# Kernel tuning notes

Measured on AMD Instinct MI355X. Metric: run time of the kernel, lower is better.

The kernel has to match this reference:

```python
import jax, jax.numpy as jnp
import numpy as np

N_NODES = 50000
N_EDGES = 800000
NODE_DIM = 128
EDGE_DIM = 32
HIDDEN = 128
OUT_DIM = 128


def _linear_params(key, fan_in, fan_out):
    k1, k2 = jax.random.split(key)
    bound = 1.0 / np.sqrt(fan_in)
    W = jax.random.uniform(k1, (fan_in, fan_out), minval=-bound, maxval=bound, dtype=jnp.float32)
    b = jax.random.uniform(k2, (fan_out,), minval=-bound, maxval=bound, dtype=jnp.float32)
    return W, b


def setup_inputs() -> dict:
    key = jax.random.key(0)
    ks = jax.random.split(key, 7)
    h = jax.random.normal(ks[0], (N_NODES, NODE_DIM), dtype=jnp.float32)
    edge_index = jax.random.randint(ks[1], (2, N_EDGES), 0, N_NODES, dtype=jnp.int64)
    edge_attr = jax.random.normal(ks[2], (N_EDGES, EDGE_DIM), dtype=jnp.float32)
    We1, be1 = _linear_params(ks[3], 2 * NODE_DIM + EDGE_DIM, HIDDEN)
    We2, be2 = _linear_params(ks[4], HIDDEN, HIDDEN)
    Wh1, bh1 = _linear_params(ks[5], NODE_DIM + HIDDEN, HIDDEN)
    Wh2, bh2 = _linear_params(ks[6], HIDDEN, OUT_DIM)
    return {"h": h, "edge_index": edge_index, "edge_attr": edge_attr,
            "We1": We1, "be1": be1, "We2": We2, "be2": be2,
            "Wh1": Wh1, "bh1": bh1, "Wh2": Wh2, "bh2": bh2}


def _mlp(x, W1, b1, W2, b2):
    return jax.nn.relu(x @ W1 + b1) @ W2 + b2


def reference(h, edge_index, edge_attr, We1, be1, We2, be2, Wh1, bh1, Wh2, bh2):
    src = edge_index[0]
    dst = edge_index[1]
    # gather endpoint features and concat with edge attributes: [E, 2*D+De]
    edge_input = jnp.concatenate([h[src], h[dst], edge_attr], axis=-1)
    m_ij = _mlp(edge_input, We1, be1, We2, be2)  # [E, H]
    # scatter-add messages into destination nodes
    m_i = jax.ops.segment_sum(m_ij, dst, num_segments=h.shape[0])  # [N, H]
    node_input = jnp.concatenate([h, m_i], axis=-1)  # [N, D+H]
    h_next = _mlp(node_input, Wh1, bh1, Wh2, bh2)  # [N, out]
    return h_next
```

## Files before the change

kernel.cpp:

```cpp
#include <hip/hip_runtime.h>

#define E_TOTAL 800000
#define N_TOTAL 50000
#define NBINS   50176

typedef __attribute__((ext_vector_type(8))) short short8;
typedef __attribute__((ext_vector_type(4))) float floatx4;

__device__ __forceinline__ unsigned short f2bf(float f) {
    union { float f; unsigned u; } x; x.f = f;
    unsigned r = x.u + 0x7fff + ((x.u >> 16) & 1);
    return (unsigned short)(r >> 16);
}

__device__ __forceinline__ void gload_lds16(const void* g, void* l) {
    __builtin_amdgcn_global_load_lds(
        (const __attribute__((address_space(1))) void*)g,
        (__attribute__((address_space(3))) void*)l, 16, 0, 0);
}
__device__ __forceinline__ void gload_lds4(const void* g, void* l) {
    __builtin_amdgcn_global_load_lds(
        (const __attribute__((address_space(1))) void*)g,
        (__attribute__((address_space(3))) void*)l, 4, 0, 0);
}

__global__ __launch_bounds__(256)
void prep(const float* __restrict__ We1, const float* __restrict__ We2,
          const float* __restrict__ Wh1, const float* __restrict__ Wh2,
          unsigned short* __restrict__ W1t, unsigned short* __restrict__ W2t,
          unsigned short* __restrict__ Wh1t, unsigned short* __restrict__ Wh2t,
          const float* __restrict__ h, unsigned short* __restrict__ hbf,
          int do_cvt, int do_sort,
          float* __restrict__ mi, int* __restrict__ hist)
{
    const int b = blockIdx.x;
    const int tid = threadIdx.x;
    if (b < 400) {
        int t = b * 256 + tid;
        if (t < 36864) {
            W1t[(t & 127) * 288 + (t >> 7)] = f2bf(We1[t]);
        } else if (t < 53248) {
            t -= 36864;
            W2t[(t & 127) * 128 + (t >> 7)] = f2bf(We2[t]);
        } else if (t < 86016) {
            t -= 53248;
            Wh1t[(t & 127) * 256 + (t >> 7)] = f2bf(Wh1[t]);
        } else if (t < 102400) {
            t -= 86016;
            Wh2t[(t & 127) * 128 + (t >> 7)] = f2bf(Wh2[t]);
        }
    } else if (b < 6650) {
        const int t = (b - 400) * 256 + tid;
        ((float4*)mi)[t] = make_float4(0.f, 0.f, 0.f, 0.f);
    } else if (b < 9775) {
        if (do_cvt) {
            const int t = (b - 6650) * 256 + tid;
            const float4* h4 = (const float4*)h;
            float4 a = h4[(size_t)t * 2];
            float4 c = h4[(size_t)t * 2 + 1];
            short8 v = { (short)f2bf(a.x), (short)f2bf(a.y), (short)f2bf(a.z), (short)f2bf(a.w),
                         (short)f2bf(c.x), (short)f2bf(c.y), (short)f2bf(c.z), (short)f2bf(c.w) };
            *(short8*)(&hbf[(size_t)t * 8]) = v;
        }
    } else {
        if (do_sort) hist[(b - 9775) * 256 + tid] = 0;
    }
}

__global__ __launch_bounds__(256) void k_hist(const int* __restrict__ ei, int* __restrict__ hist) {
    const int t = blockIdx.x * 256 + threadIdx.x;
    atomicAdd(&hist[ei[E_TOTAL + t]], 1);
}
__global__ __launch_bounds__(256) void k_scan1(const int* __restrict__ hist, int* __restrict__ partial) {
    __shared__ int s[256];
    s[threadIdx.x] = hist[blockIdx.x * 256 + threadIdx.x];
    __syncthreads();
    for (int off = 128; off > 0; off >>= 1) {
        if (threadIdx.x < off) s[threadIdx.x] += s[threadIdx.x + off];
        __syncthreads();
    }
    if (threadIdx.x == 0) partial[blockIdx.x] = s[0];
}
__global__ __launch_bounds__(256)
void k_scan2(const int* __restrict__ partial, int* __restrict__ partialOff) {
    __shared__ int s[256];
    const int t = threadIdx.x;
    const int NP = NBINS / 256;
    const int v = (t < NP) ? partial[t] : 0;
    s[t] = v; __syncthreads();
    for (int off = 1; off < 256; off <<= 1) {
        int x = (t >= off) ? s[t - off] : 0;
        __syncthreads();
        s[t] += x;
        __syncthreads();
    }
    if (t < NP) partialOff[t] = s[t] - v;
}
__global__ __launch_bounds__(256)
void k_scan3(const int* __restrict__ hist, const int* __restrict__ partialOff,
             int* __restrict__ cursor) {
    __shared__ int s[256];
    const int t = threadIdx.x, g = blockIdx.x * 256 + t;
    const int v = hist[g];
    s[t] = v; __syncthreads();
    for (int off = 1; off < 256; off <<= 1) {
        int x = (t >= off) ? s[t - off] : 0;
        __syncthreads();
        s[t] += x;
        __syncthreads();
    }
    cursor[g] = partialOff[blockIdx.x] + s[t] - v;
}
__global__ __launch_bounds__(256)
void k_scatter(const int* __restrict__ ei, const float* __restrict__ ea,
               int* __restrict__ cursor,
               int* __restrict__ srcS, int* __restrict__ dstS,
               unsigned short* __restrict__ eabf) {
    const int t = blockIdx.x * 256 + threadIdx.x;
    const int src = ei[t];
    const int dst = ei[E_TOTAL + t];
    const int pos = atomicAdd(&cursor[dst], 1);
    srcS[pos] = src;
    dstS[pos] = dst;
    const float4* ea4 = (const float4*)ea;
    #pragma unroll
    for (int j = 0; j < 4; ++j) {
        float4 a = ea4[(size_t)t * 8 + j * 2];
        float4 b = ea4[(size_t)t * 8 + j * 2 + 1];
        short8 v = { (short)f2bf(a.x), (short)f2bf(a.y), (short)f2bf(a.z), (short)f2bf(a.w),
                     (short)f2bf(b.x), (short)f2bf(b.y), (short)f2bf(b.z), (short)f2bf(b.w) };
        *(short8*)(&eabf[(size_t)pos * 32 + j * 8]) = v;
    }
}

constexpr int XK = 296;
constexpr int HK = 136;
constexpr int NK = 264;
constexpr int FJ = 132;

#define MFMA8(A, B, C) { \
    C[0][0] = __builtin_amdgcn_mfma_f32_16x16x32_bf16(A[0], B[0], C[0][0], 0, 0, 0); \
    C[0][1] = __builtin_amdgcn_mfma_f32_16x16x32_bf16(A[0], B[1], C[0][1], 0, 0, 0); \
    C[1][0] = __builtin_amdgcn_mfma_f32_16x16x32_bf16(A[1], B[0], C[1][0], 0, 0, 0); \
    C[1][1] = __builtin_amdgcn_mfma_f32_16x16x32_bf16(A[1], B[1], C[1][1], 0, 0, 0); \
    C[2][0] = __builtin_amdgcn_mfma_f32_16x16x32_bf16(A[2], B[0], C[2][0], 0, 0, 0); \
    C[2][1] = __builtin_amdgcn_mfma_f32_16x16x32_bf16(A[2], B[1], C[2][1], 0, 0, 0); \
    C[3][0] = __builtin_amdgcn_mfma_f32_16x16x32_bf16(A[3], B[0], C[3][0], 0, 0, 0); \
    C[3][1] = __builtin_amdgcn_mfma_f32_16x16x32_bf16(A[3], B[1], C[3][1], 0, 0, 0); }

__global__ __launch_bounds__(256, 2)
void edge_mfma_sorted(const unsigned short* __restrict__ hbf,
                      const int* __restrict__ srcS,
                      const int* __restrict__ dstS,
                      const unsigned short* __restrict__ eabf,
                      const unsigned short* __restrict__ W1t,
                      const float* __restrict__ b1,
                      const unsigned short* __restrict__ W2t,
                      const float* __restrict__ b2,
                      float* __restrict__ mi)
{
    constexpr int NT = E_TOTAL / 64;
    constexpr int XH = 64 * 288;
    __shared__ alignas(16) unsigned short sMem[2 * XH + 768];
    int* idb = (int*)&sMem[2 * XH];

    const int tid  = threadIdx.x;
    const int lane = tid & 63;
    const int w    = tid >> 6;
    const int q    = lane >> 4;
    const int lr   = lane & 15;
    const int n0   = w * 32;
    const int q8   = q * 8;
    const int S    = (int)gridDim.x;

    const int w1b0 = (n0 + lr) * 288, w1b1 = (n0 + 16 + lr) * 288;
    const int w2b0 = (n0 + lr) * 128, w2b1 = (n0 + 16 + lr) * 128;
    const int h0 = lr * HK, h1 = (16 + lr) * HK, h2 = (32 + lr) * HK, h3 = (48 + lr) * HK;

    const float bias1[2] = { b1[n0 + lr], b1[n0 + 16 + lr] };
    const float bias2[2] = { b2[n0 + lr], b2[n0 + 16 + lr] };

    auto ID_DMA = [&](int tt, int k) {
        if (w == 0)      gload_lds4(srcS + tt * 64 + lane, &idb[k * 128]);
        else if (w == 1) gload_lds4(dstS + tt * 64 + lane, &idb[k * 128 + 64]);
    };

    auto X_DMA = [&](int tt, int bufS, int k) {
        const int* ids = &idb[k * 128];
        #pragma unroll
        for (int j = 0; j < 9; ++j) {
            const int tj = j * 256 + tid;
            const int e  = tj / 36;
            const int p  = tj - e * 36;
            const int c  = (p < 32) ? (p ^ (e & 15)) : p;
            const int node = ids[((c & 16) ? 64 : 0) + e];
            const char* gh = (const char*)hbf + (size_t)node * 256 + (size_t)(c & 15) * 16;
            const char* ge = (const char*)eabf + ((size_t)tt * 64 + e) * 64 + (size_t)(p - 32) * 16;
            const void* g  = (p < 32) ? (const void*)gh : (const void*)ge;
            gload_lds16(g, (void*)&sMem[bufS + j * 2048 + w * 512]);
        }
    };

#define LA1(KS, A) { \
    const int cs = ((KS) < 8) ? ((((KS) * 4 + q) ^ lr) * 8) : ((32 + q) * 8); \
    A[0] = *(const short8*)(&sX[( 0 + lr) * 288 + cs]); \
    A[1] = *(const short8*)(&sX[(16 + lr) * 288 + cs]); \
    A[2] = *(const short8*)(&sX[(32 + lr) * 288 + cs]); \
    A[3] = *(const short8*)(&sX[(48 + lr) * 288 + cs]); }
#define LB1(KS, B) { B[0] = *(const short8*)(&W1t[w1b0 + (KS) * 32 + q8]); \
                     B[1] = *(const short8*)(&W1t[w1b1 + (KS) * 32 + q8]); }
#define LA2(KS, A) { A[0] = *(const short8*)(&sX[h0 + (KS) * 32 + q8]); \
                     A[1] = *(const short8*)(&sX[h1 + (KS) * 32 + q8]); \
                     A[2] = *(const short8*)(&sX[h2 + (KS) * 32 + q8]); \
                     A[3] = *(const short8*)(&sX[h3 + (KS) * 32 + q8]); }
#define LB2(KS, B) { B[0] = *(const short8*)(&W2t[w2b0 + (KS) * 32 + q8]); \
                     B[1] = *(const short8*)(&W2t[w2b1 + (KS) * 32 + q8]); }

    int t  = blockIdx.x;
    int cur = 0, ib = 0;

    ID_DMA(t, 0);
    ID_DMA(t + S, 1);
    __syncthreads();
    X_DMA(t, 0, 0);
    __syncthreads();

    while (t < NT) {
        unsigned short* sX = &sMem[cur * XH];

        const int t2 = t + 2 * S;
        if (t2 < NT) ID_DMA(t2, (ib + 2) % 3);
        const int tn = t + S;
        if (tn < NT) X_DMA(tn, (cur ^ 1) * XH, (ib + 1) % 3);

        floatx4 acc[4][2];
        #pragma unroll
        for (int mt = 0; mt < 4; ++mt)
            #pragma unroll
            for (int nt = 0; nt < 2; ++nt)
                acc[mt][nt] = (floatx4){0.f, 0.f, 0.f, 0.f};
        {
            short8 aX[4], aY[4], bX[2], bY[2];
            LB1(0, bX); LB1(1, bY); LA1(0, aX);
            LA1(1, aY); MFMA8(aX, bX, acc); LB1(2, bX);
            LA1(2, aX); MFMA8(aY, bY, acc); LB1(3, bY);
            LA1(3, aY); MFMA8(aX, bX, acc); LB1(4, bX);
            LA1(4, aX); MFMA8(aY, bY, acc); LB1(5, bY);
            LA1(5, aY); MFMA8(aX, bX, acc); LB1(6, bX);
            LA1(6, aX); MFMA8(aY, bY, acc); LB1(7, bY);
            LA1(7, aY); MFMA8(aX, bX, acc); LB1(8, bX);
            LA1(8, aX); MFMA8(aY, bY, acc);
            MFMA8(aX, bX, acc);
        }
        __syncthreads();

        {
            #pragma unroll
            for (int mt = 0; mt < 4; ++mt)
                #pragma unroll
                for (int nt = 0; nt < 2; ++nt)
                    #pragma unroll
                    for (int r = 0; r < 4; ++r) {
                        float v = fmaxf(acc[mt][nt][r] + bias1[nt], 0.f);
                        sX[(mt * 16 + q * 4 + r) * HK + n0 + nt * 16 + lr] = f2bf(v);
                    }
        }
        __syncthreads();

        floatx4 acc2[4][2];
        #pragma unroll
        for (int mt = 0; mt < 4; ++mt)
            #pragma unroll
            for (int nt = 0; nt < 2; ++nt)
                acc2[mt][nt] = (floatx4){0.f, 0.f, 0.f, 0.f};
        {
            short8 aX[4], aY[4], bX[2], bY[2];
            LB2(0, bX); LB2(1, bY); LA2(0, aX);
            LA2(1, aY); MFMA8(aX, bX, acc2); LB2(2, bX);
            LA2(2, aX); MFMA8(aY, bY, acc2); LB2(3, bY);
            LA2(3, aY); MFMA8(aX, bX, acc2);
            MFMA8(aY, bY, acc2);
        }
        __syncthreads();

        float* sF = (float*)sX;
        {
            #pragma unroll
            for (int mt = 0; mt < 4; ++mt)
                #pragma unroll
                for (int nt = 0; nt < 2; ++nt)
                    #pragma unroll
                    for (int r = 0; r < 4; ++r)
                        sF[(mt * 16 + q * 4 + r) * FJ + n0 + nt * 16 + lr] =
                            acc2[mt][nt][r] + bias2[nt];
        }
        __syncthreads();

        {
            const int* idsDst = &idb[ib * 128 + 64];
            const int g  = tid >> 7;
            const int j  = tid & 127;
            const int r0 = g * 32;
            float sum = 0.f;
            for (int r = r0; r < r0 + 32; ++r) {
                sum += sF[r * FJ + j];
                const int dst = idsDst[r];
                if (r == r0 + 31 || idsDst[r + 1] != dst) {
                    atomicAdd(&mi[(size_t)dst * 128 + j], sum);
                    sum = 0.f;
                }
            }
        }
        __syncthreads();

        cur ^= 1;
        ib = (ib == 2) ? 0 : ib + 1;
        t = tn;
    }
#undef LA1
#undef LB1
#undef LA2
#undef LB2
}

template <bool PRECVT>
__global__ __launch_bounds__(256, 8)
void edge_mfma_flat(const float* __restrict__ h,
                    const unsigned short* __restrict__ hbf,
                    const int* __restrict__ ei,
                    const float* __restrict__ ea,
                    const unsigned short* __restrict__ W1t,
                    const float* __restrict__ b1,
                    const unsigned short* __restrict__ W2t,
                    const float* __restrict__ b2,
                    float* __restrict__ mi)
{
    __shared__ unsigned short sMem[32 * XK];
    __shared__ int sDst[32];

    const int tid = threadIdx.x;
    const int e0  = blockIdx.x * 32;
    if (tid < 32) sDst[tid] = ei[E_TOTAL + e0 + tid];

    const float4* h4   = (const float4*)h;
    const short8* hbf8 = (const short8*)hbf;
    const float4* ea4  = (const float4*)ea;
    #pragma unroll
    for (int it = 0; it < 5; ++it) {
        const int idx = tid + it * 256;
        const int e  = idx / 40;
        const int c  = idx - e * 40;
        const int ge = e0 + e;
        if (c < 32) {
            const int node = (c < 16) ? ei[ge] : ei[E_TOTAL + ge];
            const int cc = c & 15;
            short8 v;
            if (PRECVT) {
                v = hbf8[(size_t)node * 16 + cc];
            } else {
                float4 x = h4[(size_t)node * 32 + cc * 2];
                float4 y = h4[(size_t)node * 32 + cc * 2 + 1];
                v = (short8){ (short)f2bf(x.x), (short)f2bf(x.y), (short)f2bf(x.z), (short)f2bf(x.w),
                              (short)f2bf(y.x), (short)f2bf(y.y), (short)f2bf(y.z), (short)f2bf(y.w) };
            }
            *(short8*)(&sMem[e * XK + c * 8]) = v;
        } else {
            float4 x = ea4[(size_t)ge * 8 + (c - 32)];
            unsigned short* p = &sMem[e * XK + 128 + c * 4];
            p[0] = f2bf(x.x); p[1] = f2bf(x.y); p[2] = f2bf(x.z); p[3] = f2bf(x.w);
        }
    }
    __syncthreads();

    const int lane = tid & 63;
    const int w    = tid >> 6;
    const int q    = lane >> 4;
    const int lr   = lane & 15;
    const int n0   = w * 32;

    floatx4 acc[2][2];
    #pragma unroll
    for (int mt = 0; mt < 2; ++mt)
        #pragma unroll
        for (int nt = 0; nt < 2; ++nt)
            acc[mt][nt] = (floatx4){0.f, 0.f, 0.f, 0.f};
    #pragma unroll
    for (int ks = 0; ks < 9; ++ks) {
        const int kb = ks * 32 + q * 8;
        short8 a[2], b[2];
        #pragma unroll
        for (int mt = 0; mt < 2; ++mt)
            a[mt] = *(const short8*)(&sMem[(mt * 16 + lr) * XK + kb]);
        #pragma unroll
        for (int nt = 0; nt < 2; ++nt)
            b[nt] = *(const short8*)(&W1t[(n0 + nt * 16 + lr) * 288 + kb]);
        #pragma unroll
        for (int mt = 0; mt < 2; ++mt)
            #pragma unroll
            for (int nt = 0; nt < 2; ++nt)
                acc[mt][nt] = __builtin_amdgcn_mfma_f32_16x16x32_bf16(
                    a[mt], b[nt], acc[mt][nt], 0, 0, 0);
    }
    __syncthreads();
    {
        float bias[2] = { b1[n0 + lr], b1[n0 + 16 + lr] };
        #pragma unroll
        for (int mt = 0; mt < 2; ++mt)
            #pragma unroll
            for (int nt = 0; nt < 2; ++nt)
                #pragma unroll
                for (int r = 0; r < 4; ++r) {
                    float v = fmaxf(acc[mt][nt][r] + bias[nt], 0.f);
                    sMem[(mt * 16 + q * 4 + r) * HK + n0 + nt * 16 + lr] = f2bf(v);
                }
    }
    __syncthreads();
    floatx4 acc2[2][2];
    #pragma unroll
    for (int mt = 0; mt < 2; ++mt)
        #pragma unroll
        for (int nt = 0; nt < 2; ++nt)
            acc2[mt][nt] = (floatx4){0.f, 0.f, 0.f, 0.f};
    #pragma unroll
    for (int ks = 0; ks < 4; ++ks) {
        const int kb = ks * 32 + q * 8;
        short8 a[2], b[2];
        #pragma unroll
        for (int mt = 0; mt < 2; ++mt)
            a[mt] = *(const short8*)(&sMem[(mt * 16 + lr) * HK + kb]);
        #pragma unroll
        for (int nt = 0; nt < 2; ++nt)
            b[nt] = *(const short8*)(&W2t[(n0 + nt * 16 + lr) * 128 + kb]);
        #pragma unroll
        for (int mt = 0; mt < 2; ++mt)
            #pragma unroll
            for (int nt = 0; nt < 2; ++nt)
                acc2[mt][nt] = __builtin_amdgcn_mfma_f32_16x16x32_bf16(
                    a[mt], b[nt], acc2[mt][nt], 0, 0, 0);
    }
    {
        float bias[2] = { b2[n0 + lr], b2[n0 + 16 + lr] };
        #pragma unroll
        for (int mt = 0; mt < 2; ++mt)
            #pragma unroll
            for (int r = 0; r < 4; ++r) {
                const int m   = mt * 16 + q * 4 + r;
                const int dst = sDst[m];
                float* row = &mi[(size_t)dst * 128];
                #pragma unroll
                for (int nt = 0; nt < 2; ++nt)
                    atomicAdd(&row[n0 + nt * 16 + lr], acc2[mt][nt][r] + bias[nt]);
            }
    }
}

template <bool USEHBF>
__global__ __launch_bounds__(256, 8)
void node_mfma(const float* __restrict__ h,
               const unsigned short* __restrict__ hbf,
               const float* __restrict__ mi,
               const unsigned short* __restrict__ W1t,
               const float* __restrict__ b1,
               const unsigned short* __restrict__ W2t,
               const float* __restrict__ b2,
               float* __restrict__ out)
{
    __shared__ unsigned short sMem[32 * NK];

    const int tid = threadIdx.x;
    const int g0  = blockIdx.x * 32;

    const float4* h4   = (const float4*)h;
    const short8* hbf8 = (const short8*)hbf;
    const float4* mi4  = (const float4*)mi;
    if (USEHBF) {
        #pragma unroll
        for (int it = 0; it < 2; ++it) {
            const int idx = tid + it * 256;
            const int n  = idx >> 4;
            const int c  = idx & 15;
            const int gn = g0 + n;
            short8 v = (short8){0,0,0,0,0,0,0,0};
            if (gn < N_TOTAL) v = hbf8[(size_t)gn * 16 + c];
            *(short8*)(&sMem[n * NK + c * 8]) = v;
        }
        #pragma unroll
        for (int it = 0; it < 4; ++it) {
            const int idx = tid + it * 256;
            const int n  = idx >> 5;
            const int c  = idx & 31;
            const int gn = g0 + n;
            float4 v = make_float4(0.f, 0.f, 0.f, 0.f);
            if (gn < N_TOTAL) v = mi4[(size_t)gn * 32 + c];
            unsigned short* p = &sMem[n * NK + 128 + c * 4];
            p[0] = f2bf(v.x); p[1] = f2bf(v.y); p[2] = f2bf(v.z); p[3] = f2bf(v.w);
        }
    } else {
        #pragma unroll
        for (int it = 0; it < 8; ++it) {
            const int idx = tid + it * 256;
            const int n  = idx >> 6;
            const int c  = idx & 63;
            const int gn = g0 + n;
            float4 v = make_float4(0.f, 0.f, 0.f, 0.f);
            if (gn < N_TOTAL)
                v = (c < 32) ? h4[(size_t)gn * 32 + c] : mi4[(size_t)gn * 32 + (c - 32)];
            unsigned short* p = &sMem[n * NK + c * 4];
            p[0] = f2bf(v.x); p[1] = f2bf(v.y); p[2] = f2bf(v.z); p[3] = f2bf(v.w);
        }
    }
    __syncthreads();

    const int lane = tid & 63;
    const int w    = tid >> 6;
    const int q    = lane >> 4;
    const int lr   = lane & 15;
    const int n0   = w * 32;

    floatx4 acc[2][2];
    #pragma unroll
    for (int mt = 0; mt < 2; ++mt)
        #pragma unroll
        for (int nt = 0; nt < 2; ++nt)
            acc[mt][nt] = (floatx4){0.f, 0.f, 0.f, 0.f};
    #pragma unroll
    for (int ks = 0; ks < 8; ++ks) {
        const int kb = ks * 32 + q * 8;
        short8 a[2], b[2];
        #pragma unroll
        for (int mt = 0; mt < 2; ++mt)
            a[mt] = *(const short8*)(&sMem[(mt * 16 + lr) * NK + kb]);
        #pragma unroll
        for (int nt = 0; nt < 2; ++nt)
            b[nt] = *(const short8*)(&W1t[(n0 + nt * 16 + lr) * 256 + kb]);
        #pragma unroll
        for (int mt = 0; mt < 2; ++mt)
            #pragma unroll
            for (int nt = 0; nt < 2; ++nt)
                acc[mt][nt] = __builtin_amdgcn_mfma_f32_16x16x32_bf16(
                    a[mt], b[nt], acc[mt][nt], 0, 0, 0);
    }
    __syncthreads();
    {
        float bias[2] = { b1[n0 + lr], b1[n0 + 16 + lr] };
        #pragma unroll
        for (int mt = 0; mt < 2; ++mt)
            #pragma unroll
            for (int nt = 0; nt < 2; ++nt)
                #pragma unroll
                for (int r = 0; r < 4; ++r) {
                    float v = fmaxf(acc[mt][nt][r] + bias[nt], 0.f);
                    sMem[(mt * 16 + q * 4 + r) * HK + n0 + nt * 16 + lr] = f2bf(v);
                }
    }
    __syncthreads();
    floatx4 acc2[2][2];
    #pragma unroll
    for (int mt = 0; mt < 2; ++mt)
        #pragma unroll
        for (int nt = 0; nt < 2; ++nt)
            acc2[mt][nt] = (floatx4){0.f, 0.f, 0.f, 0.f};
    #pragma unroll
    for (int ks = 0; ks < 4; ++ks) {
        const int kb = ks * 32 + q * 8;
        short8 a[2], b[2];
        #pragma unroll
        for (int mt = 0; mt < 2; ++mt)
            a[mt] = *(const short8*)(&sMem[(mt * 16 + lr) * HK + kb]);
        #pragma unroll
        for (int nt = 0; nt < 2; ++nt)
            b[nt] = *(const short8*)(&W2t[(n0 + nt * 16 + lr) * 128 + kb]);
        #pragma unroll
        for (int mt = 0; mt < 2; ++mt)
            #pragma unroll
            for (int nt = 0; nt < 2; ++nt)
                acc2[mt][nt] = __builtin_amdgcn_mfma_f32_16x16x32_bf16(
                    a[mt], b[nt], acc2[mt][nt], 0, 0, 0);
    }
    {
        float bias[2] = { b2[n0 + lr], b2[n0 + 16 + lr] };
        #pragma unroll
        for (int mt = 0; mt < 2; ++mt)
            #pragma unroll
            for (int r = 0; r < 4; ++r) {
                const int gm = g0 + mt * 16 + q * 4 + r;
                if (gm < N_TOTAL) {
                    #pragma unroll
                    for (int nt = 0; nt < 2; ++nt)
                        out[(size_t)gm * 128 + n0 + nt * 16 + lr] =
                            acc2[mt][nt][r] + bias[nt];
                }
            }
    }
}

extern "C" void kernel_launch(void* const* d_in, const int* in_sizes, int n_in,
                              void* d_out, int out_size, void* d_ws, size_t ws_size,
                              hipStream_t stream) {
    const float* h   = (const float*)d_in[0];
    const int*   ei  = (const int*)d_in[1];
    const float* ea  = (const float*)d_in[2];
    const float* We1 = (const float*)d_in[3];
    const float* be1 = (const float*)d_in[4];
    const float* We2 = (const float*)d_in[5];
    const float* be2 = (const float*)d_in[6];
    const float* Wh1 = (const float*)d_in[7];
    const float* bh1 = (const float*)d_in[8];
    const float* Wh2 = (const float*)d_in[9];
    const float* bh2 = (const float*)d_in[10];
    float* out = (float*)d_out;

    const size_t szMi   = (size_t)N_TOTAL * 128 * sizeof(float);
    const size_t szW1t  = 128 * 288 * 2;
    const size_t szW2t  = 128 * 128 * 2;
    const size_t szWh1t = 128 * 256 * 2;
    const size_t szWh2t = 128 * 128 * 2;
    const size_t szHbf  = (size_t)N_TOTAL * 128 * 2;
    const size_t szIds  = (size_t)E_TOTAL * 4;
    const size_t szEabf = (size_t)E_TOTAL * 32 * 2;
    const size_t szHist = (size_t)NBINS * 4;

    const size_t offW1t  = szMi;
    const size_t offW2t  = offW1t + szW1t;
    const size_t offWh1t = offW2t + szW2t;
    const size_t offWh2t = offWh1t + szWh1t;
    const size_t offHbf  = offWh2t + szWh2t;
    const size_t offSrc  = offHbf + szHbf;
    const size_t offDst  = offSrc + szIds;
    const size_t offEabf = offDst + szIds;
    const size_t offHist = offEabf + szEabf;
    const size_t offCur  = offHist + szHist;
    const size_t offP1   = offCur + szHist;
    const size_t offP2   = offP1 + 1024;
    const size_t needFull = offP2 + 1024;
    const size_t needCvt  = offSrc;

    char* wsb = (char*)d_ws;
    float* mi = (float*)wsb;
    unsigned short* W1t  = (unsigned short*)(wsb + offW1t);
    unsigned short* W2t  = (unsigned short*)(wsb + offW2t);
    unsigned short* Wh1t = (unsigned short*)(wsb + offWh1t);
    unsigned short* Wh2t = (unsigned short*)(wsb + offWh2t);
    unsigned short* hbf  = (unsigned short*)(wsb + offHbf);
    int* srcS    = (int*)(wsb + offSrc);
    int* dstS    = (int*)(wsb + offDst);
    unsigned short* eabf = (unsigned short*)(wsb + offEabf);
    int* hist    = (int*)(wsb + offHist);
    int* cursor  = (int*)(wsb + offCur);
    int* partial = (int*)(wsb + offP1);
    int* poff    = (int*)(wsb + offP2);

    const int full   = (ws_size >= needFull) ? 1 : 0;
    const int do_cvt = (ws_size >= needCvt + szHbf) ? 1 : 0;

    prep<<<9971, 256, 0, stream>>>(We1, We2, Wh1, Wh2, W1t, W2t, Wh1t, Wh2t,
                                   h, hbf, do_cvt, full, mi, hist);

    if (full) {
        k_hist<<<E_TOTAL / 256, 256, 0, stream>>>(ei, hist);
        k_scan1<<<NBINS / 256, 256, 0, stream>>>(hist, partial);
        k_scan2<<<1, 256, 0, stream>>>(partial, poff);
        k_scan3<<<NBINS / 256, 256, 0, stream>>>(hist, poff, cursor);
        k_scatter<<<E_TOTAL / 256, 256, 0, stream>>>(ei, ea, cursor, srcS, dstS, eabf);
        edge_mfma_sorted<<<512, 256, 0, stream>>>(
            hbf, srcS, dstS, eabf, W1t, be1, W2t, be2, mi);
        node_mfma<true><<<(N_TOTAL + 31) / 32, 256, 0, stream>>>(
            h, hbf, mi, Wh1t, bh1, Wh2t, bh2, out);
    } else if (do_cvt) {
        edge_mfma_flat<true><<<E_TOTAL / 32, 256, 0, stream>>>(
            h, hbf, ei, ea, W1t, be1, W2t, be2, mi);
        node_mfma<true><<<(N_TOTAL + 31) / 32, 256, 0, stream>>>(
            h, hbf, mi, Wh1t, bh1, Wh2t, bh2, out);
    } else {
        edge_mfma_flat<false><<<E_TOTAL / 32, 256, 0, stream>>>(
            h, nullptr, ei, ea, W1t, be1, W2t, be2, mi);
        node_mfma<false><<<(N_TOTAL + 31) / 32, 256, 0, stream>>>(
            h, nullptr, mi, Wh1t, bh1, Wh2t, bh2, out);
    }
    (void)in_sizes; (void)n_in; (void)out_size;
}
```

Baseline: 443.4 us.

## Use 8 waves per block in sorted edge kernel, 16 output columns each

Doubles the edge MLP kernel's block size from 256 to 512 threads. Each of the 8 waves now computes a 16-column slice of the hidden output instead of 32, with the gather DMA, epilogue and segmented atomic reduction rebalanced across the larger block. The aim is more waves per CU to hide gather latency and spread the per-tile work, at the cost of each wave re-reading the A tile from LDS, since A-operand LDS traffic per tile doubles. Launch bounds now request 4 blocks of 512 threads per CU, which tightens the register budget.

```diff
diff --git a/kernel.cpp b/kernel.cpp
--- a/kernel.cpp
+++ b/kernel.cpp
@@ -148,7 +148,13 @@
     C[3][0] = __builtin_amdgcn_mfma_f32_16x16x32_bf16(A[3], B[0], C[3][0], 0, 0, 0); \
     C[3][1] = __builtin_amdgcn_mfma_f32_16x16x32_bf16(A[3], B[1], C[3][1], 0, 0, 0); }
 
-__global__ __launch_bounds__(256, 2)
+#define MFMA4(A, B, C) { \
+    C[0] = __builtin_amdgcn_mfma_f32_16x16x32_bf16(A[0], B, C[0], 0, 0, 0); \
+    C[1] = __builtin_amdgcn_mfma_f32_16x16x32_bf16(A[1], B, C[1], 0, 0, 0); \
+    C[2] = __builtin_amdgcn_mfma_f32_16x16x32_bf16(A[2], B, C[2], 0, 0, 0); \
+    C[3] = __builtin_amdgcn_mfma_f32_16x16x32_bf16(A[3], B, C[3], 0, 0, 0); }
+
+__global__ __launch_bounds__(512, 4)
 void edge_mfma_sorted(const unsigned short* __restrict__ hbf,
                       const int* __restrict__ srcS,
                       const int* __restrict__ dstS,
@@ -169,16 +175,16 @@
     const int w    = tid >> 6;
     const int q    = lane >> 4;
     const int lr   = lane & 15;
-    const int n0   = w * 32;
+    const int n0   = w * 16;
     const int q8   = q * 8;
     const int S    = (int)gridDim.x;
 
-    const int w1b0 = (n0 + lr) * 288, w1b1 = (n0 + 16 + lr) * 288;
-    const int w2b0 = (n0 + lr) * 128, w2b1 = (n0 + 16 + lr) * 128;
+    const int w1b = (n0 + lr) * 288;
+    const int w2b = (n0 + lr) * 128;
     const int h0 = lr * HK, h1 = (16 + lr) * HK, h2 = (32 + lr) * HK, h3 = (48 + lr) * HK;
 
-    const float bias1[2] = { b1[n0 + lr], b1[n0 + 16 + lr] };
-    const float bias2[2] = { b2[n0 + lr], b2[n0 + 16 + lr] };
+    const float bias1 = b1[n0 + lr];
+    const float bias2 = b2[n0 + lr];
 
     auto ID_DMA = [&](int tt, int k) {
         if (w == 0)      gload_lds4(srcS + tt * 64 + lane, &idb[k * 128]);
@@ -188,16 +194,18 @@
     auto X_DMA = [&](int tt, int bufS, int k) {
         const int* ids = &idb[k * 128];
         #pragma unroll
-        for (int j = 0; j < 9; ++j) {
-            const int tj = j * 256 + tid;
-            const int e  = tj / 36;
-            const int p  = tj - e * 36;
-            const int c  = (p < 32) ? (p ^ (e & 15)) : p;
-            const int node = ids[((c & 16) ? 64 : 0) + e];
-            const char* gh = (const char*)hbf + (size_t)node * 256 + (size_t)(c & 15) * 16;
-            const char* ge = (const char*)eabf + ((size_t)tt * 64 + e) * 64 + (size_t)(p - 32) * 16;
-            const void* g  = (p < 32) ? (const void*)gh : (const void*)ge;
-            gload_lds16(g, (void*)&sMem[bufS + j * 2048 + w * 512]);
+        for (int j = 0; j < 5; ++j) {
+            if (j < 4 || tid < 256) {
+                const int tj = j * 512 + tid;
+                const int e  = tj / 36;
+                const int p  = tj - e * 36;
+                const int c  = (p < 32) ? (p ^ (e & 15)) : p;
+                const int node = ids[((c & 16) ? 64 : 0) + e];
+                const char* gh = (const char*)hbf + (size_t)node * 256 + (size_t)(c & 15) * 16;
+                const char* ge = (const char*)eabf + ((size_t)tt * 64 + e) * 64 + (size_t)(p - 32) * 16;
+                const void* g  = (p < 32) ? (const void*)gh : (const void*)ge;
+                gload_lds16(g, (void*)&sMem[bufS + j * 4096 + w * 512]);
+            }
         }
     };
 
@@ -207,14 +215,12 @@
     A[1] = *(const short8*)(&sX[(16 + lr) * 288 + cs]); \
     A[2] = *(const short8*)(&sX[(32 + lr) * 288 + cs]); \
     A[3] = *(const short8*)(&sX[(48 + lr) * 288 + cs]); }
-#define LB1(KS, B) { B[0] = *(const short8*)(&W1t[w1b0 + (KS) * 32 + q8]); \
-                     B[1] = *(const short8*)(&W1t[w1b1 + (KS) * 32 + q8]); }
+#define LB1(KS, B) { B = *(const short8*)(&W1t[w1b + (KS) * 32 + q8]); }
 #define LA2(KS, A) { A[0] = *(const short8*)(&sX[h0 + (KS) * 32 + q8]); \
                      A[1] = *(const short8*)(&sX[h1 + (KS) * 32 + q8]); \
                      A[2] = *(const short8*)(&sX[h2 + (KS) * 32 + q8]); \
                      A[3] = *(const short8*)(&sX[h3 + (KS) * 32 + q8]); }
-#define LB2(KS, B) { B[0] = *(const short8*)(&W2t[w2b0 + (KS) * 32 + q8]); \
-                     B[1] = *(const short8*)(&W2t[w2b1 + (KS) * 32 + q8]); }
+#define LB2(KS, B) { B = *(const short8*)(&W2t[w2b + (KS) * 32 + q8]); }
 
     int t  = blockIdx.x;
     int cur = 0, ib = 0;
@@ -233,24 +239,22 @@
         const int tn = t + S;
         if (tn < NT) X_DMA(tn, (cur ^ 1) * XH, (ib + 1) % 3);
 
-        floatx4 acc[4][2];
+        floatx4 acc[4];
         #pragma unroll
         for (int mt = 0; mt < 4; ++mt)
-            #pragma unroll
-            for (int nt = 0; nt < 2; ++nt)
-                acc[mt][nt] = (floatx4){0.f, 0.f, 0.f, 0.f};
+            acc[mt] = (floatx4){0.f, 0.f, 0.f, 0.f};
         {
-            short8 aX[4], aY[4], bX[2], bY[2];
+            short8 aX[4], aY[4], bX, bY;
             LB1(0, bX); LB1(1, bY); LA1(0, aX);
-            LA1(1, aY); MFMA8(aX, bX, acc); LB1(2, bX);
-            LA1(2, aX); MFMA8(aY, bY, acc); LB1(3, bY);
-            LA1(3, aY); MFMA8(aX, bX, acc); LB1(4, bX);
-            LA1(4, aX); MFMA8(aY, bY, acc); LB1(5, bY);
-            LA1(5, aY); MFMA8(aX, bX, acc); LB1(6, bX);
-            LA1(6, aX); MFMA8(aY, bY, acc); LB1(7, bY);
-            LA1(7, aY); MFMA8(aX, bX, acc); LB1(8, bX);
-            LA1(8, aX); MFMA8(aY, bY, acc);
-            MFMA8(aX, bX, acc);
+            LA1(1, aY); MFMA4(aX, bX, acc); LB1(2, bX);
+            LA1(2, aX); MFMA4(aY, bY, acc); LB1(3, bY);
+            LA1(3, aY); MFMA4(aX, bX, acc); LB1(4, bX);
+            LA1(4, aX); MFMA4(aY, bY, acc); LB1(5, bY);
+            LA1(5, aY); MFMA4(aX, bX, acc); LB1(6, bX);
+            LA1(6, aX); MFMA4(aY, bY, acc); LB1(7, bY);
+            LA1(7, aY); MFMA4(aX, bX, acc); LB1(8, bX);
+            LA1(8, aX); MFMA4(aY, bY, acc);
+            MFMA4(aX, bX, acc);
         }
         __syncthreads();
 
@@ -258,28 +262,24 @@
             #pragma unroll
             for (int mt = 0; mt < 4; ++mt)
                 #pragma unroll
-                for (int nt = 0; nt < 2; ++nt)
-                    #pragma unroll
-                    for (int r = 0; r < 4; ++r) {
-                        float v = fmaxf(acc[mt][nt][r] + bias1[nt], 0.f);
-                        sX[(mt * 16 + q * 4 + r) * HK + n0 + nt * 16 + lr] = f2bf(v);
-                    }
-        }
-        __syncthreads();
-
-        floatx4 acc2[4][2];
+                for (int r = 0; r < 4; ++r) {
+                    float v = fmaxf(acc[mt][r] + bias1, 0.f);
+                    sX[(mt * 16 + q * 4 + r) * HK + n0 + lr] = f2bf(v);
+                }
+        }
+        __syncthreads();
+
+        floatx4 acc2[4];
         #pragma unroll
         for (int mt = 0; mt < 4; ++mt)
-            #pragma unroll
-            for (int nt = 0; nt < 2; ++nt)
-                acc2[mt][nt] = (floatx4){0.f, 0.f, 0.f, 0.f};
+            acc2[mt] = (floatx4){0.f, 0.f, 0.f, 0.f};
         {
-            short8 aX[4], aY[4], bX[2], bY[2];
+            short8 aX[4], aY[4], bX, bY;
             LB2(0, bX); LB2(1, bY); LA2(0, aX);
-            LA2(1, aY); MFMA8(aX, bX, acc2); LB2(2, bX);
-            LA2(2, aX); MFMA8(aY, bY, acc2); LB2(3, bY);
-            LA2(3, aY); MFMA8(aX, bX, acc2);
-            MFMA8(aY, bY, acc2);
+            LA2(1, aY); MFMA4(aX, bX, acc2); LB2(2, bX);
+            LA2(2, aX); MFMA4(aY, bY, acc2); LB2(3, bY);
+            LA2(3, aY); MFMA4(aX, bX, acc2);
+            MFMA4(aY, bY, acc2);
         }
         __syncthreads();
 
@@ -288,11 +288,8 @@
             #pragma unroll
             for (int mt = 0; mt < 4; ++mt)
                 #pragma unroll
-                for (int nt = 0; nt < 2; ++nt)
-                    #pragma unroll
-                    for (int r = 0; r < 4; ++r)
-                        sF[(mt * 16 + q * 4 + r) * FJ + n0 + nt * 16 + lr] =
-                            acc2[mt][nt][r] + bias2[nt];
+                for (int r = 0; r < 4; ++r)
+                    sF[(mt * 16 + q * 4 + r) * FJ + n0 + lr] = acc2[mt][r] + bias2;
         }
         __syncthreads();
 
@@ -300,12 +297,12 @@
             const int* idsDst = &idb[ib * 128 + 64];
             const int g  = tid >> 7;
             const int j  = tid & 127;
-            const int r0 = g * 32;
+            const int r0 = g * 16;
             float sum = 0.f;
-            for (int r = r0; r < r0 + 32; ++r) {
+            for (int r = r0; r < r0 + 16; ++r) {
                 sum += sF[r * FJ + j];
                 const int dst = idsDst[r];
-                if (r == r0 + 31 || idsDst[r + 1] != dst) {
+                if (r == r0 + 15 || idsDst[r + 1] != dst) {
                     atomicAdd(&mi[(size_t)dst * 128 + j], sum);
                     sum = 0.f;
                 }
@@ -662,7 +659,7 @@
         k_scan2<<<1, 256, 0, stream>>>(partial, poff);
         k_scan3<<<NBINS / 256, 256, 0, stream>>>(hist, poff, cursor);
         k_scatter<<<E_TOTAL / 256, 256, 0, stream>>>(ei, ea, cursor, srcS, dstS, eabf);
-        edge_mfma_sorted<<<512, 256, 0, stream>>>(
+        edge_mfma_sorted<<<512, 512, 0, stream>>>(
             hbf, srcS, dstS, eabf, W1t, be1, W2t, be2, mi);
         node_mfma<true><<<(N_TOTAL + 31) / 32, 256, 0, stream>>>(
             h, hbf, mi, Wh1t, bh1, Wh2t, bh2, out);
```

Result: slower. 483.7 us (+9.1%).

## Split edge tile across eight waves with 2x4 wave grid per block

Applied to the files above, without the earlier changes.

Doubles the edge kernel block size to 512 threads. Waves are arranged as 2 row groups by 4 column groups, so each wave computes a 32x32 output tile instead of 64x32. The gather DMA and the segmented scatter-add loop are re-partitioned to match: 5 DMA rounds, and 16-row segments across 4 thread groups. This is meant to add latency hiding through more waves per block. In exchange, each weight fragment is loaded twice per tile, shorter segments issue more atomics, and the tighter launch bound may pressure registers.

```diff
diff --git a/kernel.cpp b/kernel.cpp
--- a/kernel.cpp
+++ b/kernel.cpp
@@ -138,17 +138,13 @@
 constexpr int NK = 264;
 constexpr int FJ = 132;
 
-#define MFMA8(A, B, C) { \
+#define MFMA22(A, B, C) { \
     C[0][0] = __builtin_amdgcn_mfma_f32_16x16x32_bf16(A[0], B[0], C[0][0], 0, 0, 0); \
     C[0][1] = __builtin_amdgcn_mfma_f32_16x16x32_bf16(A[0], B[1], C[0][1], 0, 0, 0); \
     C[1][0] = __builtin_amdgcn_mfma_f32_16x16x32_bf16(A[1], B[0], C[1][0], 0, 0, 0); \
-    C[1][1] = __builtin_amdgcn_mfma_f32_16x16x32_bf16(A[1], B[1], C[1][1], 0, 0, 0); \
-    C[2][0] = __builtin_amdgcn_mfma_f32_16x16x32_bf16(A[2], B[0], C[2][0], 0, 0, 0); \
-    C[2][1] = __builtin_amdgcn_mfma_f32_16x16x32_bf16(A[2], B[1], C[2][1], 0, 0, 0); \
-    C[3][0] = __builtin_amdgcn_mfma_f32_16x16x32_bf16(A[3], B[0], C[3][0], 0, 0, 0); \
-    C[3][1] = __builtin_amdgcn_mfma_f32_16x16x32_bf16(A[3], B[1], C[3][1], 0, 0, 0); }
-
-__global__ __launch_bounds__(256, 2)
+    C[1][1] = __builtin_amdgcn_mfma_f32_16x16x32_bf16(A[1], B[1], C[1][1], 0, 0, 0); }
+
+__global__ __launch_bounds__(512, 4)
 void edge_mfma_sorted(const unsigned short* __restrict__ hbf,
                       const int* __restrict__ srcS,
                       const int* __restrict__ dstS,
@@ -167,15 +163,19 @@
     const int tid  = threadIdx.x;
     const int lane = tid & 63;
     const int w    = tid >> 6;
+    const int rg   = w >> 2;
+    const int cg   = w & 3;
     const int q    = lane >> 4;
     const int lr   = lane & 15;
-    const int n0   = w * 32;
+    const int m0   = rg * 32;
+    const int n0   = cg * 32;
     const int q8   = q * 8;
     const int S    = (int)gridDim.x;
 
     const int w1b0 = (n0 + lr) * 288, w1b1 = (n0 + 16 + lr) * 288;
     const int w2b0 = (n0 + lr) * 128, w2b1 = (n0 + 16 + lr) * 128;
-    const int h0 = lr * HK, h1 = (16 + lr) * HK, h2 = (32 + lr) * HK, h3 = (48 + lr) * HK;
+    const int a0r = m0 + lr, a1r = m0 + 16 + lr;
+    const int h0 = a0r * HK, h1 = a1r * HK;
 
     const float bias1[2] = { b1[n0 + lr], b1[n0 + 16 + lr] };
     const float bias2[2] = { b2[n0 + lr], b2[n0 + 16 + lr] };
@@ -188,31 +188,29 @@
     auto X_DMA = [&](int tt, int bufS, int k) {
         const int* ids = &idb[k * 128];
         #pragma unroll
-        for (int j = 0; j < 9; ++j) {
-            const int tj = j * 256 + tid;
-            const int e  = tj / 36;
-            const int p  = tj - e * 36;
-            const int c  = (p < 32) ? (p ^ (e & 15)) : p;
-            const int node = ids[((c & 16) ? 64 : 0) + e];
-            const char* gh = (const char*)hbf + (size_t)node * 256 + (size_t)(c & 15) * 16;
-            const char* ge = (const char*)eabf + ((size_t)tt * 64 + e) * 64 + (size_t)(p - 32) * 16;
-            const void* g  = (p < 32) ? (const void*)gh : (const void*)ge;
-            gload_lds16(g, (void*)&sMem[bufS + j * 2048 + w * 512]);
+        for (int j = 0; j < 5; ++j) {
+            if (j < 4 || tid < 256) {
+                const int tj = j * 512 + tid;
+                const int e  = tj / 36;
+                const int p  = tj - e * 36;
+                const int c  = (p < 32) ? (p ^ (e & 15)) : p;
+                const int node = ids[((c & 16) ? 64 : 0) + e];
+                const char* gh = (const char*)hbf + (size_t)node * 256 + (size_t)(c & 15) * 16;
+                const char* ge = (const char*)eabf + ((size_t)tt * 64 + e) * 64 + (size_t)(p - 32) * 16;
+                const void* g  = (p < 32) ? (const void*)gh : (const void*)ge;
+                gload_lds16(g, (void*)&sMem[bufS + j * 4096 + w * 512]);
+            }
         }
     };
 
 #define LA1(KS, A) { \
     const int cs = ((KS) < 8) ? ((((KS) * 4 + q) ^ lr) * 8) : ((32 + q) * 8); \
-    A[0] = *(const short8*)(&sX[( 0 + lr) * 288 + cs]); \
-    A[1] = *(const short8*)(&sX[(16 + lr) * 288 + cs]); \
-    A[2] = *(const short8*)(&sX[(32 + lr) * 288 + cs]); \
-    A[3] = *(const short8*)(&sX[(48 + lr) * 288 + cs]); }
+    A[0] = *(const short8*)(&sX[a0r * 288 + cs]); \
+    A[1] = *(const short8*)(&sX[a1r * 288 + cs]); }
 #define LB1(KS, B) { B[0] = *(const short8*)(&W1t[w1b0 + (KS) * 32 + q8]); \
                      B[1] = *(const short8*)(&W1t[w1b1 + (KS) * 32 + q8]); }
 #define LA2(KS, A) { A[0] = *(const short8*)(&sX[h0 + (KS) * 32 + q8]); \
-                     A[1] = *(const short8*)(&sX[h1 + (KS) * 32 + q8]); \
-                     A[2] = *(const short8*)(&sX[h2 + (KS) * 32 + q8]); \
-                     A[3] = *(const short8*)(&sX[h3 + (KS) * 32 + q8]); }
+                     A[1] = *(const short8*)(&sX[h1 + (KS) * 32 + q8]); }
 #define LB2(KS, B) { B[0] = *(const short8*)(&W2t[w2b0 + (KS) * 32 + q8]); \
                      B[1] = *(const short8*)(&W2t[w2b1 + (KS) * 32 + q8]); }
 
@@ -233,65 +231,65 @@
         const int tn = t + S;
         if (tn < NT) X_DMA(tn, (cur ^ 1) * XH, (ib + 1) % 3);
 
-        floatx4 acc[4][2];
-        #pragma unroll
-        for (int mt = 0; mt < 4; ++mt)
+        floatx4 acc[2][2];
+        #pragma unroll
+        for (int mt = 0; mt < 2; ++mt)
             #pragma unroll
             for (int nt = 0; nt < 2; ++nt)
                 acc[mt][nt] = (floatx4){0.f, 0.f, 0.f, 0.f};
         {
-            short8 aX[4], aY[4], bX[2], bY[2];
+            short8 aX[2], aY[2], bX[2], bY[2];
             LB1(0, bX); LB1(1, bY); LA1(0, aX);
-            LA1(1, aY); MFMA8(aX, bX, acc); LB1(2, bX);
-            LA1(2, aX); MFMA8(aY, bY, acc); LB1(3, bY);
-            LA1(3, aY); MFMA8(aX, bX, acc); LB1(4, bX);
-            LA1(4, aX); MFMA8(aY, bY, acc); LB1(5, bY);
-            LA1(5, aY); MFMA8(aX, bX, acc); LB1(6, bX);
-            LA1(6, aX); MFMA8(aY, bY, acc); LB1(7, bY);
-            LA1(7, aY); MFMA8(aX, bX, acc); LB1(8, bX);
-            LA1(8, aX); MFMA8(aY, bY, acc);
-            MFMA8(aX, bX, acc);
+            LA1(1, aY); MFMA22(aX, bX, acc); LB1(2, bX);
+            LA1(2, aX); MFMA22(aY, bY, acc); LB1(3, bY);
+            LA1(3, aY); MFMA22(aX, bX, acc); LB1(4, bX);
+            LA1(4, aX); MFMA22(aY, bY, acc); LB1(5, bY);
+            LA1(5, aY); MFMA22(aX, bX, acc); LB1(6, bX);
+            LA1(6, aX); MFMA22(aY, bY, acc); LB1(7, bY);
+            LA1(7, aY); MFMA22(aX, bX, acc); LB1(8, bX);
+            LA1(8, aX); MFMA22(aY, bY, acc);
+            MFMA22(aX, bX, acc);
         }
         __syncthreads();
 
         {
             #pragma unroll
-            for (int mt = 0; mt < 4; ++mt)
+            for (int mt = 0; mt < 2; ++mt)
                 #pragma unroll
                 for (int nt = 0; nt < 2; ++nt)
                     #pragma unroll
                     for (int r = 0; r < 4; ++r) {
                         float v = fmaxf(acc[mt][nt][r] + bias1[nt], 0.f);
-                        sX[(mt * 16 + q * 4 + r) * HK + n0 + nt * 16 + lr] = f2bf(v);
+                        sX[(m0 + mt * 16 + q * 4 + r) * HK + n0 + nt * 16 + lr] = f2bf(v);
                     }
         }
         __syncthreads();
 
-        floatx4 acc2[4][2];
-        #pragma unroll
-        for (int mt = 0; mt < 4; ++mt)
+        floatx4 acc2[2][2];
+        #pragma unroll
+        for (int mt = 0; mt < 2; ++mt)
             #pragma unroll
             for (int nt = 0; nt < 2; ++nt)
                 acc2[mt][nt] = (floatx4){0.f, 0.f, 0.f, 0.f};
         {
-            short8 aX[4], aY[4], bX[2], bY[2];
+            short8 aX[2], aY[2], bX[2], bY[2];
             LB2(0, bX); LB2(1, bY); LA2(0, aX);
-            LA2(1, aY); MFMA8(aX, bX, acc2); LB2(2, bX);
-            LA2(2, aX); MFMA8(aY, bY, acc2); LB2(3, bY);
-            LA2(3, aY); MFMA8(aX, bX, acc2);
-            MFMA8(aY, bY, acc2);
+            LA2(1, aY); MFMA22(aX, bX, acc2); LB2(2, bX);
+            LA2(2, aX); MFMA22(aY, bY, acc2); LB2(3, bY);
+            LA2(3, aY); MFMA22(aX, bX, acc2);
+            MFMA22(aY, bY, acc2);
         }
         __syncthreads();
 
         float* sF = (float*)sX;
         {
             #pragma unroll
-            for (int mt = 0; mt < 4; ++mt)
+            for (int mt = 0; mt < 2; ++mt)
                 #pragma unroll
                 for (int nt = 0; nt < 2; ++nt)
                     #pragma unroll
                     for (int r = 0; r < 4; ++r)
-                        sF[(mt * 16 + q * 4 + r) * FJ + n0 + nt * 16 + lr] =
+                        sF[(m0 + mt * 16 + q * 4 + r) * FJ + n0 + nt * 16 + lr] =
                             acc2[mt][nt][r] + bias2[nt];
         }
         __syncthreads();
@@ -300,12 +298,12 @@
             const int* idsDst = &idb[ib * 128 + 64];
             const int g  = tid >> 7;
             const int j  = tid & 127;
-            const int r0 = g * 32;
+            const int r0 = g * 16;
             float sum = 0.f;
-            for (int r = r0; r < r0 + 32; ++r) {
+            for (int r = r0; r < r0 + 16; ++r) {
                 sum += sF[r * FJ + j];
                 const int dst = idsDst[r];
-                if (r == r0 + 31 || idsDst[r + 1] != dst) {
+                if (r == r0 + 15 || idsDst[r + 1] != dst) {
                     atomicAdd(&mi[(size_t)dst * 128 + j], sum);
                     sum = 0.f;
                 }
@@ -662,7 +660,7 @@
         k_scan2<<<1, 256, 0, stream>>>(partial, poff);
         k_scan3<<<NBINS / 256, 256, 0, stream>>>(hist, poff, cursor);
         k_scatter<<<E_TOTAL / 256, 256, 0, stream>>>(ei, ea, cursor, srcS, dstS, eabf);
-        edge_mfma_sorted<<<512, 256, 0, stream>>>(
+        edge_mfma_sorted<<<512, 512, 0, stream>>>(
             hbf, srcS, dstS, eabf, W1t, be1, W2t, be2, mi);
         node_mfma<true><<<(N_TOTAL + 31) / 32, 256, 0, stream>>>(
             h, hbf, mi, Wh1t, bh1, Wh2t, bh2, out);
```

Result: slower. 610.4 us (+37.7%).
